# Optimization experiments

Hardware: AMD Instinct MI355X
Metric: run time of the kernel (lower is better)

Reference implementation:

```python
import jax, jax.numpy as jnp
import numpy as np

K_ORDER = 3  # spline order k from init_kwargs


def get_spline_basis(x_ext, grid, k):
    # x_ext: (n, batch), grid: (n, G+2k+1)
    grid = grid[:, :, None]          # (n, P, 1)
    x = x_ext[:, None, :]            # (n, 1, batch)
    # order-0 indicator bases
    bases = ((x >= grid[:, :-1]) & (x < grid[:, 1:])).astype(x_ext.dtype)
    # Cox-de Boor recursion up to order k
    for K in range(1, k + 1):
        left = (x - grid[:, :-(K + 1)]) / (grid[:, K:-1] - grid[:, :-(K + 1)])
        right = (grid[:, K + 1:] - x) / (grid[:, K + 1:] - grid[:, 1:-K])
        bases = left * bases[:, :-1] + right * bases[:, 1:]
    return bases  # (n, G+k, batch)


def setup_inputs() -> dict:
    key = jax.random.key(0)
    k1, k2 = jax.random.split(key)
    n_in, n_out, batch, k = 64, 64, 2048, K_ORDER
    n = n_in * n_out
    init_G = 3
    h = 2.0 / init_G  # (1 - (-1)) / init_G
    grid_row = jnp.arange(-k, init_G + k + 1, dtype=jnp.float32) * h - 1.0  # (G+2k+1,) = (10,)
    grid = jnp.tile(grid_row[None, :], (n, 1))                              # (n, 10)
    x = jax.random.normal(k1, (batch, n_in), dtype=jnp.float32)
    c_basis = 0.1 * jax.random.normal(k2, (n, init_G + k), dtype=jnp.float32)  # (n, 6)
    c_spl = jnp.ones((n,), dtype=jnp.float32)
    c_res = jnp.ones((n,), dtype=jnp.float32)
    return {"x": x, "c_basis": c_basis, "c_spl": c_spl, "c_res": c_res, "grid": grid}


def reference(x, c_basis, c_spl, c_res, grid):
    batch, n_in = x.shape
    n = grid.shape[0]
    n_out = n // n_in
    # replicate each input across n_out outgoing edges: flat index = out*n_in + in
    x_ext = jnp.broadcast_to(x[:, None, :], (batch, n_out, n_in)).reshape(batch, n).T  # (n, batch)
    # residual branch: swish
    res = (x_ext * jax.nn.sigmoid(x_ext)).T  # (batch, n)
    # spline branch
    Bi = get_spline_basis(x_ext, grid, K_ORDER)        # (n, G+k, batch)
    spl = jnp.einsum('ij,ijk->ki', c_basis, Bi)        # (batch, n)
    y = c_spl[None, :] * spl + c_res[None, :] * res    # (batch, n)
    y = y.reshape(batch, n_out, n_in).sum(axis=2) / n_in  # (batch, n_out)
    # spline regularization term
    grid_r = grid.reshape(n_out, n_in, -1)
    input_norm = grid_r[:, :, -1] - grid_r[:, :, 0] + 1e-05
    spl_reg = jnp.mean(jnp.abs(spl.reshape(batch, n_out, n_in)), axis=0) / input_norm  # (n_out, n_in)
    return (y, spl_reg)
```

## Files before the change

kernel.cpp:

```cpp
#include <hip/hip_runtime.h>
#include <math.h>


#define BATCHN 2048
#define NI     64
#define NO     64
#define NTOTAL 4096
#define BB     8
#define NCHUNK (BATCHN / BB)
#define TPB    512

__device__ __forceinline__ void eval_basis6(float xv,
                                            const float* tt,
                                            const float* inv1,
                                            const float* inv2,
                                            const float* inv3,
                                            float* bout, float* silu)
{
    float c[10], d[10];
#pragma unroll
    for (int m = 0; m < 10; ++m) {
        c[m] = (xv >= tt[m]) ? 1.0f : 0.0f;
        d[m] = xv - tt[m];
    }
    float b[9], w[9];
#pragma unroll
    for (int m = 0; m < 9; ++m) b[m] = c[m] - c[m + 1];
#pragma unroll
    for (int m = 0; m < 9; ++m) w[m] = b[m] * inv1[m];
#pragma unroll
    for (int m = 0; m < 8; ++m) b[m] = d[m] * w[m] - d[m + 2] * w[m + 1];
#pragma unroll
    for (int m = 0; m < 8; ++m) w[m] = b[m] * inv2[m];
#pragma unroll
    for (int m = 0; m < 7; ++m) b[m] = d[m] * w[m] - d[m + 3] * w[m + 1];
#pragma unroll
    for (int m = 0; m < 7; ++m) w[m] = b[m] * inv3[m];
#pragma unroll
    for (int m = 0; m < 6; ++m) bout[m] = d[m] * w[m] - d[m + 4] * w[m + 1];
    *silu = xv / (1.0f + expf(-xv));
}

__global__ __launch_bounds__(TPB, 2) void kan_main(
    const float* __restrict__ x, const float* __restrict__ cb,
    const float* __restrict__ c_spl, const float* __restrict__ c_res,
    const float* __restrict__ grid, float* __restrict__ y,
    float* __restrict__ regpart, int write_part)
{
    __shared__ float sB[7][512];
    const int t    = threadIdx.x;
    const int lane = t & 63;
    const int wv   = t >> 6;
    const int bchunk = blockIdx.x;
    const int bbase  = bchunk * BB;

    float tt[10];
#pragma unroll
    for (int m = 0; m < 10; ++m) tt[m] = grid[m];
    float inv1[9], inv2[8], inv3[7];
#pragma unroll
    for (int m = 0; m < 9; ++m) inv1[m] = 1.0f / (tt[m + 1] - tt[m]);
#pragma unroll
    for (int m = 0; m < 8; ++m) inv2[m] = 1.0f / (tt[m + 2] - tt[m]);
#pragma unroll
    for (int m = 0; m < 7; ++m) inv3[m] = 1.0f / (tt[m + 3] - tt[m]);

    {
        const float xv = x[bbase * NI + t];
        float bo[6], sl;
        eval_basis6(xv, tt, inv1, inv2, inv3, bo, &sl);
#pragma unroll
        for (int m = 0; m < 6; ++m) sB[m][t] = bo[m];
        sB[6][t] = sl;
    }
    __syncthreads();

    float B0[8], B1[8], B2[8], B3[8], B4[8], B5[8], SL[8];
#pragma unroll
    for (int bb = 0; bb < 8; ++bb) {
        const int p = bb * 64 + lane;
        B0[bb] = sB[0][p]; B1[bb] = sB[1][p]; B2[bb] = sB[2][p];
        B3[bb] = sB[3][p]; B4[bb] = sB[4][p]; B5[bb] = sB[5][p];
        SL[bb] = sB[6][p];
    }

    const bool p0 = (lane & 1), p1 = (lane & 2), p2 = (lane & 4);
#pragma unroll
    for (int jj = 0; jj < 8; ++jj) {
        const int j = jj * TPB + t;
        const float* cbp = cb + j * 6;
        const float2 c01 = *(const float2*)(cbp);
        const float2 c23 = *(const float2*)(cbp + 2);
        const float2 c45 = *(const float2*)(cbp + 4);
        const float cs = c_spl[j];
        const float cr = c_res[j];

        float v[8];
        float rabs = 0.0f;
#pragma unroll
        for (int bb = 0; bb < 8; ++bb) {
            float s = c01.x * B0[bb];
            s = fmaf(c01.y, B1[bb], s);
            s = fmaf(c23.x, B2[bb], s);
            s = fmaf(c23.y, B3[bb], s);
            s = fmaf(c45.x, B4[bb], s);
            s = fmaf(c45.y, B5[bb], s);
            rabs += fabsf(s);
            v[bb] = fmaf(cs, s, cr * SL[bb]);
        }
        if (write_part) regpart[bchunk * NTOTAL + j] = rabs;

#pragma unroll
        for (int r = 0; r < 4; ++r) {
            float send = p0 ? v[r] : v[r + 4];
            float recv = __shfl_xor(send, 1, 64);
            float keep = p0 ? v[r + 4] : v[r];
            v[r] = keep + recv;
        }
#pragma unroll
        for (int r = 0; r < 2; ++r) {
            float send = p1 ? v[r] : v[r + 2];
            float recv = __shfl_xor(send, 2, 64);
            float keep = p1 ? v[r + 2] : v[r];
            v[r] = keep + recv;
        }
        {
            float send = p2 ? v[0] : v[1];
            float recv = __shfl_xor(send, 4, 64);
            float keep = p2 ? v[1] : v[0];
            v[0] = keep + recv;
        }
        v[0] += __shfl_xor(v[0], 8, 64);
        v[0] += __shfl_xor(v[0], 16, 64);
        v[0] += __shfl_xor(v[0], 32, 64);
        if (lane < 8) {
            const int bbL = ((lane & 1) << 2) | (lane & 2) | ((lane >> 2) & 1);
            const int o = jj * 8 + wv;
            y[(bbase + bbL) * NO + o] = v[0] * (1.0f / 64.0f);
        }
    }
}

__global__ __launch_bounds__(256) void kan_reduce(
    const float* __restrict__ regpart, const float* __restrict__ grid,
    float* __restrict__ outreg)
{
    __shared__ float sR[4][64];
    const int t = threadIdx.x;
    const int qo = t & 63, gs = t >> 6;
    const int q = blockIdx.x * 64 + qo;
    float s = 0.0f;
#pragma unroll 16
    for (int g = gs * 64; g < gs * 64 + 64; ++g) s += regpart[g * NTOTAL + q];
    sR[gs][qo] = s;
    __syncthreads();
    if (t < 64) {
        const float tot = sR[0][qo] + sR[1][qo] + sR[2][qo] + sR[3][qo];
        const float norm = grid[q * 10 + 9] - grid[q * 10] + 1e-5f;
        outreg[q] = (tot * (1.0f / (float)BATCHN)) / norm;
    }
}

__global__ __launch_bounds__(256) void kan_reg_standalone(
    const float* __restrict__ x, const float* __restrict__ cb,
    const float* __restrict__ grid, float* __restrict__ outreg)
{
    __shared__ float sB2[6][256];
    __shared__ float sR[256];
    const int t = threadIdx.x;
    const int i = blockIdx.x;

    float tt[10];
#pragma unroll
    for (int m = 0; m < 10; ++m) tt[m] = grid[m];
    float inv1[9], inv2[8], inv3[7];
#pragma unroll
    for (int m = 0; m < 9; ++m) inv1[m] = 1.0f / (tt[m + 1] - tt[m]);
#pragma unroll
    for (int m = 0; m < 8; ++m) inv2[m] = 1.0f / (tt[m + 2] - tt[m]);
#pragma unroll
    for (int m = 0; m < 7; ++m) inv3[m] = 1.0f / (tt[m + 3] - tt[m]);

    const int o = t >> 2;
    const int q = t & 3;
    const int j = o * NI + i;
    const float c0 = cb[j * 6 + 0], c1 = cb[j * 6 + 1], c2 = cb[j * 6 + 2];
    const float c3 = cb[j * 6 + 3], c4 = cb[j * 6 + 4], c5 = cb[j * 6 + 5];

    float acc = 0.0f;
    for (int tile = 0; tile < 8; ++tile) {
        const float xv = x[(tile * 256 + t) * NI + i];
        float bo[6], sl;
        eval_basis6(xv, tt, inv1, inv2, inv3, bo, &sl);
        __syncthreads();
#pragma unroll
        for (int m = 0; m < 6; ++m) sB2[m][t] = bo[m];
        __syncthreads();
        for (int bi = 0; bi < 64; ++bi) {
            const int b = q * 64 + ((bi + q * 8) & 63);
            float s = c0 * sB2[0][b];
            s = fmaf(c1, sB2[1][b], s);
            s = fmaf(c2, sB2[2][b], s);
            s = fmaf(c3, sB2[3][b], s);
            s = fmaf(c4, sB2[4][b], s);
            s = fmaf(c5, sB2[5][b], s);
            acc += fabsf(s);
        }
    }
    sR[t] = acc;
    __syncthreads();
    if (t < 64) {
        const float s = sR[t * 4 + 0] + sR[t * 4 + 1] + sR[t * 4 + 2] + sR[t * 4 + 3];
        const int jj = t * NI + i;
        const float norm = grid[jj * 10 + 9] - grid[jj * 10] + 1e-5f;
        outreg[jj] = (s * (1.0f / (float)BATCHN)) / norm;
    }
}

extern "C" void kernel_launch(void* const* d_in, const int* in_sizes, int n_in,
                              void* d_out, int out_size, void* d_ws, size_t ws_size,
                              hipStream_t stream) {
    (void)in_sizes; (void)n_in; (void)out_size;
    const float* x    = (const float*)d_in[0];
    const float* cb   = (const float*)d_in[1];
    const float* cspl = (const float*)d_in[2];
    const float* cres = (const float*)d_in[3];
    const float* grid = (const float*)d_in[4];
    float* y      = (float*)d_out;
    float* outreg = y + BATCHN * NO;

    const size_t needed = (size_t)NCHUNK * NTOTAL * sizeof(float);
    if (ws_size >= needed) {
        float* part = (float*)d_ws;
        kan_main<<<NCHUNK, TPB, 0, stream>>>(x, cb, cspl, cres, grid, y, part, 1);
        kan_reduce<<<NTOTAL / 64, 256, 0, stream>>>(part, grid, outreg);
    } else {
        kan_main<<<NCHUNK, TPB, 0, stream>>>(x, cb, cspl, cres, grid, y,
                                             (float*)d_ws, 0);
        kan_reg_standalone<<<NI, 256, 0, stream>>>(x, cb, grid, outreg);
    }
}
```

Measured before the change: 74.10 us.

## Replace partial-sum workspace and reduce kernel with atomic accumulation

The main kernel now adds each chunk's normalized absolute-spline sum straight into the regularization output with atomicAdd, after a memset zeroes it. This removes the workspace writes, the second reduce kernel launch and the pass that reads the partials back. In exchange there are 256 atomic adds per output element, which can contend, and the summation order is no longer deterministic. The kernel also adds a per-edge grid load for the norm.

```diff
diff --git a/kernel.cpp b/kernel.cpp
--- a/kernel.cpp
+++ b/kernel.cpp
@@ -45,7 +45,7 @@
     const float* __restrict__ x, const float* __restrict__ cb,
     const float* __restrict__ c_spl, const float* __restrict__ c_res,
     const float* __restrict__ grid, float* __restrict__ y,
-    float* __restrict__ regpart, int write_part)
+    float* __restrict__ outreg)
 {
     __shared__ float sB[7][512];
     const int t    = threadIdx.x;
@@ -108,7 +108,10 @@
             rabs += fabsf(s);
             v[bb] = fmaf(cs, s, cr * SL[bb]);
         }
-        if (write_part) regpart[bchunk * NTOTAL + j] = rabs;
+        {
+            const float norm = grid[j * 10 + 9] - grid[j * 10] + 1e-5f;
+            atomicAdd(&outreg[j], rabs * (1.0f / (float)BATCHN) / norm);
+        }
 
 #pragma unroll
         for (int r = 0; r < 4; ++r) {
@@ -141,86 +144,10 @@
     }
 }
 
-__global__ __launch_bounds__(256) void kan_reduce(
-    const float* __restrict__ regpart, const float* __restrict__ grid,
-    float* __restrict__ outreg)
-{
-    __shared__ float sR[4][64];
-    const int t = threadIdx.x;
-    const int qo = t & 63, gs = t >> 6;
-    const int q = blockIdx.x * 64 + qo;
-    float s = 0.0f;
-#pragma unroll 16
-    for (int g = gs * 64; g < gs * 64 + 64; ++g) s += regpart[g * NTOTAL + q];
-    sR[gs][qo] = s;
-    __syncthreads();
-    if (t < 64) {
-        const float tot = sR[0][qo] + sR[1][qo] + sR[2][qo] + sR[3][qo];
-        const float norm = grid[q * 10 + 9] - grid[q * 10] + 1e-5f;
-        outreg[q] = (tot * (1.0f / (float)BATCHN)) / norm;
-    }
-}
-
-__global__ __launch_bounds__(256) void kan_reg_standalone(
-    const float* __restrict__ x, const float* __restrict__ cb,
-    const float* __restrict__ grid, float* __restrict__ outreg)
-{
-    __shared__ float sB2[6][256];
-    __shared__ float sR[256];
-    const int t = threadIdx.x;
-    const int i = blockIdx.x;
-
-    float tt[10];
-#pragma unroll
-    for (int m = 0; m < 10; ++m) tt[m] = grid[m];
-    float inv1[9], inv2[8], inv3[7];
-#pragma unroll
-    for (int m = 0; m < 9; ++m) inv1[m] = 1.0f / (tt[m + 1] - tt[m]);
-#pragma unroll
-    for (int m = 0; m < 8; ++m) inv2[m] = 1.0f / (tt[m + 2] - tt[m]);
-#pragma unroll
-    for (int m = 0; m < 7; ++m) inv3[m] = 1.0f / (tt[m + 3] - tt[m]);
-
-    const int o = t >> 2;
-    const int q = t & 3;
-    const int j = o * NI + i;
-    const float c0 = cb[j * 6 + 0], c1 = cb[j * 6 + 1], c2 = cb[j * 6 + 2];
-    const float c3 = cb[j * 6 + 3], c4 = cb[j * 6 + 4], c5 = cb[j * 6 + 5];
-
-    float acc = 0.0f;
-    for (int tile = 0; tile < 8; ++tile) {
-        const float xv = x[(tile * 256 + t) * NI + i];
-        float bo[6], sl;
-        eval_basis6(xv, tt, inv1, inv2, inv3, bo, &sl);
-        __syncthreads();
-#pragma unroll
-        for (int m = 0; m < 6; ++m) sB2[m][t] = bo[m];
-        __syncthreads();
-        for (int bi = 0; bi < 64; ++bi) {
-            const int b = q * 64 + ((bi + q * 8) & 63);
-            float s = c0 * sB2[0][b];
-            s = fmaf(c1, sB2[1][b], s);
-            s = fmaf(c2, sB2[2][b], s);
-            s = fmaf(c3, sB2[3][b], s);
-            s = fmaf(c4, sB2[4][b], s);
-            s = fmaf(c5, sB2[5][b], s);
-            acc += fabsf(s);
-        }
-    }
-    sR[t] = acc;
-    __syncthreads();
-    if (t < 64) {
-        const float s = sR[t * 4 + 0] + sR[t * 4 + 1] + sR[t * 4 + 2] + sR[t * 4 + 3];
-        const int jj = t * NI + i;
-        const float norm = grid[jj * 10 + 9] - grid[jj * 10] + 1e-5f;
-        outreg[jj] = (s * (1.0f / (float)BATCHN)) / norm;
-    }
-}
-
 extern "C" void kernel_launch(void* const* d_in, const int* in_sizes, int n_in,
                               void* d_out, int out_size, void* d_ws, size_t ws_size,
                               hipStream_t stream) {
-    (void)in_sizes; (void)n_in; (void)out_size;
+    (void)in_sizes; (void)n_in; (void)out_size; (void)d_ws; (void)ws_size;
     const float* x    = (const float*)d_in[0];
     const float* cb   = (const float*)d_in[1];
     const float* cspl = (const float*)d_in[2];
@@ -229,14 +156,6 @@
     float* y      = (float*)d_out;
     float* outreg = y + BATCHN * NO;
 
-    const size_t needed = (size_t)NCHUNK * NTOTAL * sizeof(float);
-    if (ws_size >= needed) {
-        float* part = (float*)d_ws;
-        kan_main<<<NCHUNK, TPB, 0, stream>>>(x, cb, cspl, cres, grid, y, part, 1);
-        kan_reduce<<<NTOTAL / 64, 256, 0, stream>>>(part, grid, outreg);
-    } else {
-        kan_main<<<NCHUNK, TPB, 0, stream>>>(x, cb, cspl, cres, grid, y,
-                                             (float*)d_ws, 0);
-        kan_reg_standalone<<<NI, 256, 0, stream>>>(x, cb, grid, outreg);
-    }
+    hipMemsetAsync(outreg, 0, NTOTAL * sizeof(float), stream);
+    kan_main<<<NCHUNK, TPB, 0, stream>>>(x, cb, cspl, cres, grid, y, outreg);
 }
```

Measured after the change: 78.36 us. 5.7% more time.
